# Performance work log

Hardware: AMD Instinct MI355X
Metric: run time of the kernel (lower is better)

Reference implementation:

```python
import jax, jax.numpy as jnp
import numpy as np

D = 768  # in_channels == out_channels (forced by residual + shared LayerNorm)
B, S = 8, 2048


def setup_inputs() -> dict:
    key = jax.random.key(0)
    ks = jax.random.split(key, 5)
    x = jax.random.normal(ks[0], (B, S, D), dtype=jnp.float32)
    # LayerNorm params
    ln_g = jnp.ones((D,), dtype=jnp.float32)
    ln_b = jnp.zeros((D,), dtype=jnp.float32)
    # Q/K linear params (torch Linear: y = x @ W.T + b)
    scale = 1.0 / np.sqrt(D)
    Wq = jax.random.uniform(ks[1], (D, D), jnp.float32, -scale, scale)
    bq = jax.random.uniform(ks[2], (D,), jnp.float32, -scale, scale)
    Wk = jax.random.uniform(ks[3], (D, D), jnp.float32, -scale, scale)
    bk = jax.random.uniform(ks[4], (D,), jnp.float32, -scale, scale)
    return {"x": x, "ln_g": ln_g, "ln_b": ln_b, "Wq": Wq, "bq": bq, "Wk": Wk, "bk": bk}


def _layernorm(x, g, b, eps=1e-5):
    mu = jnp.mean(x, axis=-1, keepdims=True)
    var = jnp.mean(jnp.square(x - mu), axis=-1, keepdims=True)
    return (x - mu) * jax.lax.rsqrt(var + eps) * g + b


def reference(x, ln_g, ln_b, Wq, bq, Wk, bk):
    origin = x
    xn = _layernorm(x, ln_g, ln_b)
    Q = xn @ Wq.T + bq  # [B,S,D]
    K = xn @ Wk.T + bk  # [B,S,D]
    scores = jnp.einsum('bsd,btd->bst', Q, K) / jnp.sqrt(jnp.asarray(D, x.dtype))
    attn = jax.nn.softmax(scores, axis=-1)  # [B,S,S]
    out = jnp.einsum('bst,btd->bsd', attn, origin) + origin
    # note: original then computes relu(layernorm(out)) but returns `out` (dead code)
    return out
```

## Files before the change

### kernel.cpp

```cpp
#include <hip/hip_runtime.h>

typedef __bf16 bf16;
typedef __bf16 v8bf __attribute__((ext_vector_type(8)));
typedef __bf16 v4bf __attribute__((ext_vector_type(4)));
typedef float  v4f  __attribute__((ext_vector_type(4)));

__device__ __forceinline__ void gload_lds16(const void* g, void* l) {
    __builtin_amdgcn_global_load_lds(
        (const __attribute__((address_space(1))) void*)g,
        (__attribute__((address_space(3))) void*)l, 16, 0, 0);
}

__global__ __launch_bounds__(256)
void ln_cast(const float* __restrict__ x, const float* __restrict__ g,
             const float* __restrict__ b, bf16* __restrict__ xn,
             bf16* __restrict__ xv, float* __restrict__ L)
{
    const long row = blockIdx.x;
    const float* xr = x + row * 768;
    const int tid = threadIdx.x;
    const int wave = tid >> 6, lane = tid & 63;

    if (row < 64) L[row * 256 + tid] = 0.0f;

    float a0 = xr[tid], a1 = xr[tid + 256], a2 = xr[tid + 512];
    float s = a0 + a1 + a2;
    #pragma unroll
    for (int off = 32; off; off >>= 1) s += __shfl_xor(s, off);
    __shared__ float sh[4], sh2[4];
    if (!lane) sh[wave] = s;
    __syncthreads();
    const float mu = (sh[0] + sh[1] + sh[2] + sh[3]) * (1.0f / 768.0f);

    float d0 = a0 - mu, d1 = a1 - mu, d2 = a2 - mu;
    float ss = d0 * d0 + d1 * d1 + d2 * d2;
    #pragma unroll
    for (int off = 32; off; off >>= 1) ss += __shfl_xor(ss, off);
    if (!lane) sh2[wave] = ss;
    __syncthreads();
    const float var = (sh2[0] + sh2[1] + sh2[2] + sh2[3]) * (1.0f / 768.0f);
    const float rstd = rsqrtf(var + 1e-5f);

    bf16* xnr = xn + row * 768;
    bf16* xvr = xv + row * 768;
    xnr[tid]       = (bf16)(d0 * rstd * g[tid]       + b[tid]);
    xnr[tid + 256] = (bf16)(d1 * rstd * g[tid + 256] + b[tid + 256]);
    xnr[tid + 512] = (bf16)(d2 * rstd * g[tid + 512] + b[tid + 512]);
    xvr[tid]       = (bf16)a0;
    xvr[tid + 256] = (bf16)a1;
    xvr[tid + 512] = (bf16)a2;
}

__global__ __launch_bounds__(256)
void cvt_w(const float* __restrict__ Wq, const float* __restrict__ Wk,
           bf16* __restrict__ Wcat)
{
    const int z = blockIdx.y;
    const float* src = z ? Wk : Wq;
    bf16* dst = Wcat + (long)z * 768 * 768;
    const int i = (blockIdx.x * 256 + threadIdx.x) * 4;
    const float4 v = *(const float4*)(src + i);
    v4bf o = {(bf16)v.x, (bf16)v.y, (bf16)v.z, (bf16)v.w};
    *(v4bf*)(dst + i) = o;
}

__global__ __launch_bounds__(256)
void transpose_bf(const bf16* __restrict__ in, bf16* __restrict__ outT)
{
    __shared__ __attribute__((aligned(16))) bf16 tile[64 * 64];
    const int t0 = blockIdx.x * 64, d0 = blockIdx.y * 64;
    in   += (long)blockIdx.z * 2048 * 768;
    outT += (long)blockIdx.z * 768 * 2048;
    const int tid = threadIdx.x;

    #pragma unroll
    for (int it = 0; it < 2; ++it) {
        const int lin = it * 256 + tid;
        const int r = lin >> 3;
        const int g = lin & 7;
        const int pg = g ^ (r & 7) ^ ((r >> 3) & 7);
        v8bf v = *(const v8bf*)(in + (long)(t0 + r) * 768 + d0 + g * 8);
        *(v8bf*)(tile + r * 64 + pg * 8) = v;
    }
    __syncthreads();
    #pragma unroll
    for (int it = 0; it < 2; ++it) {
        const int lin = it * 256 + tid;
        const int dd = lin >> 3;
        const int tb = lin & 7;
        v8bf o;
        #pragma unroll
        for (int j = 0; j < 8; ++j) {
            const int t = tb * 8 + j;
            const int pg = (dd >> 3) ^ (t & 7) ^ ((t >> 3) & 7);
            o[j] = tile[t * 64 + pg * 8 + (dd & 7)];
        }
        *(v8bf*)(outT + (long)(d0 + dd) * 2048 + t0 + tb * 8) = o;
    }
}

__global__ __launch_bounds__(256)
void gemm_qk(const bf16* __restrict__ A, const bf16* __restrict__ W,
             const float* __restrict__ bq, const float* __restrict__ bk,
             float qscale, bf16* __restrict__ Qb, bf16* __restrict__ Kb)
{
    __shared__ __attribute__((aligned(16))) bf16 As[2][128 * 32];
    __shared__ __attribute__((aligned(16))) bf16 Bs[2][128 * 32];

    const int bx = blockIdx.x;
    const int r = bx & 7, j = bx >> 3;
    const int m0 = (r * 16 + j / 12) * 128;
    const int n0 = (j % 12) * 128;

    const int tid = threadIdx.x, wave = tid >> 6, lane = tid & 63;
    const bf16* Ab = A + (long)m0 * 768;
    const bf16* Bb = W + (long)n0 * 768;

    const int lrow = lane >> 2;
    const int lk   = (lane & 3) * 8;
    const int wm = (wave >> 1) * 64, wn = (wave & 1) * 64;
    const int lr = lane & 15, lq = lane >> 4;

    v4f acc[4][4] = {};

    for (int kk = 0; kk < 768; kk += 64) {
        #pragma unroll
        for (int p = 0; p < 2; ++p)
            #pragma unroll
            for (int it = 0; it < 2; ++it) {
                const int c = it * 4 + wave;
                const int row = c * 16 + lrow;
                gload_lds16(Ab + (long)row * 768 + kk + p * 32 + lk,
                            (char*)As[p] + c * 1024);
                gload_lds16(Bb + (long)row * 768 + kk + p * 32 + lk,
                            (char*)Bs[p] + c * 1024);
            }
        __syncthreads();

        #pragma unroll
        for (int p = 0; p < 2; ++p) {
            v8bf af[4], bfr[4];
            #pragma unroll
            for (int i = 0; i < 4; ++i)
                af[i] = *(const v8bf*)(As[p] + (wm + i * 16 + lr) * 32 + lq * 8);
            #pragma unroll
            for (int jj = 0; jj < 4; ++jj)
                bfr[jj] = *(const v8bf*)(Bs[p] + (wn + jj * 16 + lr) * 32 + lq * 8);
            #pragma unroll
            for (int i = 0; i < 4; ++i)
                #pragma unroll
                for (int jj = 0; jj < 4; ++jj)
                    acc[i][jj] = __builtin_amdgcn_mfma_f32_16x16x32_bf16(
                        af[i], bfr[jj], acc[i][jj], 0, 0, 0);
        }
        __syncthreads();
    }

    const bool isQ = (n0 < 768);
    const float* bias = isQ ? bq : bk;
    const float sc = isQ ? qscale : 1.0f;
    bf16* C = isQ ? Qb : Kb;
    const int c0 = isQ ? n0 : n0 - 768;

    #pragma unroll
    for (int i = 0; i < 4; ++i) {
        #pragma unroll
        for (int rr = 0; rr < 4; ++rr) {
            const int row = m0 + wm + i * 16 + lq * 4 + rr;
            #pragma unroll
            for (int jj = 0; jj < 4; ++jj) {
                const int col = c0 + wn + jj * 16 + lr;
                C[(long)row * 768 + col] = (bf16)((acc[i][jj][rr] + bias[col]) * sc);
            }
        }
    }
}

__global__ __launch_bounds__(512, 2)
void gemm_scores(const bf16* __restrict__ Q, const bf16* __restrict__ K,
                 bf16* __restrict__ E, float* __restrict__ L)
{
    __shared__ __attribute__((aligned(16))) bf16 lds[3][24576];

    const int bx = blockIdx.x;
    const int batch = bx & 7, j = bx >> 3;
    const int mt = j >> 3, nt = j & 7;
    const int m0 = mt * 128, n0 = nt * 256;

    const bf16* Ag = Q + (long)batch * 2048 * 768 + (long)m0 * 768;
    const bf16* Bg = K + (long)batch * 2048 * 768 + (long)n0 * 768;
    bf16* C = E + (long)batch * 2048 * 2048;
    float* Lb = L + (long)batch * 2048;

    const int tid = threadIdx.x, wv = tid >> 6, lane = tid & 63;
    const int wr = wv >> 2, wc = wv & 3;
    const int lr = lane & 15, lq = lane >> 4;

    auto stageA = [&](int slot, int kk, int a) {
        const int lin = a * 64 + lane;
        const int r = lin >> 3;
        const int ck = (lin & 7) ^ (r & 7);
        gload_lds16(Ag + (long)r * 768 + kk + ck * 8,
                    (char*)lds[slot] + a * 1024);
    };
    auto stageB = [&](int slot, int kk, int b) {
        const int lin = b * 64 + lane;
        const int r = lin >> 3;
        const int ck = (lin & 7) ^ (r & 7);
        gload_lds16(Bg + (long)r * 768 + kk + ck * 8,
                    (char*)lds[slot] + 16384 + b * 1024);
    };

    v4f acc[4][4] = {};
    const int NT = 12;

    #pragma unroll
    for (int tt = 0; tt < 2; ++tt) {
        stageA(tt, tt * 64, wv * 2 + 0);
        stageA(tt, tt * 64, wv * 2 + 1);
        #pragma unroll
        for (int l = 0; l < 4; ++l) stageB(tt, tt * 64, wv * 4 + l);
    }
    asm volatile("s_waitcnt vmcnt(6)" ::: "memory");
    __builtin_amdgcn_s_barrier();

    for (int t = 0; t < NT; ++t) {
        const int cur = t % 3;
        const int nxt = (t + 2) % 3;
        const int kk2 = (t + 2) * 64;
        const bf16* As = lds[cur];
        const bf16* Bs = lds[cur] + 8192;
        const bool pre = (t + 2 < NT);

        v8bf af[4][2], bfr[2][2];
        #pragma unroll
        for (int i = 0; i < 4; ++i) {
            const int row = wr * 64 + i * 16 + lr;
            #pragma unroll
            for (int s = 0; s < 2; ++s)
                af[i][s] = *(const v8bf*)(As + row * 64 +
                                          (((s * 4 + lq) ^ (row & 7)) << 3));
        }
        #pragma unroll
        for (int jn = 0; jn < 2; ++jn) {
            const int row = wc * 64 + jn * 16 + lr;
            #pragma unroll
            for (int s = 0; s < 2; ++s)
                bfr[jn][s] = *(const v8bf*)(Bs + row * 64 +
                                            (((s * 4 + lq) ^ (row & 7)) << 3));
        }
        if (pre) {
            stageA(nxt, kk2, wv * 2 + 0);
            stageA(nxt, kk2, wv * 2 + 1);
            stageB(nxt, kk2, wv * 4 + 0);
        }
        __builtin_amdgcn_s_barrier();
        asm volatile("s_waitcnt lgkmcnt(0)" ::: "memory");
        __builtin_amdgcn_s_setprio(1);
        #pragma unroll
        for (int s = 0; s < 2; ++s)
            #pragma unroll
            for (int i = 0; i < 4; ++i)
                #pragma unroll
                for (int jn = 0; jn < 2; ++jn)
                    acc[i][jn] = __builtin_amdgcn_mfma_f32_16x16x32_bf16(
                        af[i][s], bfr[jn][s], acc[i][jn], 0, 0, 0);
        __builtin_amdgcn_s_setprio(0);
        __builtin_amdgcn_s_barrier();

        #pragma unroll
        for (int jn = 0; jn < 2; ++jn) {
            const int row = wc * 64 + (jn + 2) * 16 + lr;
            #pragma unroll
            for (int s = 0; s < 2; ++s)
                bfr[jn][s] = *(const v8bf*)(Bs + row * 64 +
                                            (((s * 4 + lq) ^ (row & 7)) << 3));
        }
        if (pre) {
            stageB(nxt, kk2, wv * 4 + 1);
            stageB(nxt, kk2, wv * 4 + 2);
            stageB(nxt, kk2, wv * 4 + 3);
        }
        __builtin_amdgcn_s_barrier();
        asm volatile("s_waitcnt lgkmcnt(0)" ::: "memory");
        __builtin_amdgcn_s_setprio(1);
        #pragma unroll
        for (int s = 0; s < 2; ++s)
            #pragma unroll
            for (int i = 0; i < 4; ++i)
                #pragma unroll
                for (int jn = 0; jn < 2; ++jn)
                    acc[i][jn + 2] = __builtin_amdgcn_mfma_f32_16x16x32_bf16(
                        af[i][s], bfr[jn][s], acc[i][jn + 2], 0, 0, 0);
        __builtin_amdgcn_s_setprio(0);
        if (t < NT - 2)       asm volatile("s_waitcnt vmcnt(6)" ::: "memory");
        else if (t == NT - 2) asm volatile("s_waitcnt vmcnt(0)" ::: "memory");
        __builtin_amdgcn_s_barrier();
    }

    #pragma unroll
    for (int i = 0; i < 4; ++i) {
        #pragma unroll
        for (int rr = 0; rr < 4; ++rr) {
            const int row = m0 + wr * 64 + i * 16 + lq * 4 + rr;
            float e[4], rs = 0.f;
            #pragma unroll
            for (int jn = 0; jn < 4; ++jn) {
                e[jn] = __expf(acc[i][jn][rr]);
                rs += e[jn];
            }
            #pragma unroll
            for (int off = 1; off < 16; off <<= 1) rs += __shfl_xor(rs, off);
            if (lr == 0) atomicAdd(&Lb[row], rs);
            #pragma unroll
            for (int jn = 0; jn < 4; ++jn) {
                const int col = n0 + wc * 64 + jn * 16 + lr;
                C[(long)row * 2048 + col] = (bf16)e[jn];
            }
        }
    }
}

__global__ __launch_bounds__(512, 2)
void gemm_pv(const bf16* __restrict__ P, const bf16* __restrict__ VT,
             const float* __restrict__ L, const float* __restrict__ Xres,
             float* __restrict__ Out)
{
    __shared__ __attribute__((aligned(16))) bf16 lds[2][32768];

    const int bx = blockIdx.x;
    const int batch = bx & 7, j = bx >> 3;
    const int m0 = (j >> 1) * 128;
    const int n0 = (j & 1) * 384;

    const bf16* Ag = P  + (long)batch * 2048 * 2048 + (long)m0 * 2048;
    const bf16* Bg = VT + (long)batch * 768 * 2048  + (long)n0 * 2048;
    const float* Lb = L + (long)batch * 2048;
    const float* Xr = Xres + (long)batch * 2048 * 768;
    float* O = Out + (long)batch * 2048 * 768;

    const int tid = threadIdx.x, wv = tid >> 6, lane = tid & 63;
    const int wr = wv >> 2, wc = wv & 3;
    const int lr = lane & 15, lq = lane >> 4;

    auto stageA = [&](int slot, int kk, int a) {
        const int lin = a * 64 + lane;
        const int r = lin >> 3;
        const int ck = (lin & 7) ^ (r & 7);
        gload_lds16(Ag + (long)r * 2048 + kk + ck * 8,
                    (char*)lds[slot] + a * 1024);
    };
    auto stageB = [&](int slot, int kk, int b) {
        const int lin = b * 64 + lane;
        const int r = lin >> 3;
        const int ck = (lin & 7) ^ (r & 7);
        gload_lds16(Bg + (long)r * 2048 + kk + ck * 8,
                    (char*)lds[slot] + 16384 + b * 1024);
    };

    v4f acc[4][6] = {};
    const int NT = 32;

    stageA(0, 0, wv * 2 + 0);
    stageA(0, 0, wv * 2 + 1);
    #pragma unroll
    for (int l = 0; l < 6; ++l) stageB(0, 0, wv * 6 + l);
    asm volatile("s_waitcnt vmcnt(0)" ::: "memory");
    __builtin_amdgcn_s_barrier();

    for (int t = 0; t < NT; ++t) {
        const int cur = t & 1, nxt = cur ^ 1;
        const int kk1 = (t + 1) * 64;
        const bf16* As = lds[cur];
        const bf16* Bs = lds[cur] + 8192;
        const bool pre = (t + 1 < NT);

        v8bf af[4][2], bfr[3][2];
        #pragma unroll
        for (int i = 0; i < 4; ++i) {
            const int row = wr * 64 + i * 16 + lr;
            #pragma unroll
            for (int s = 0; s < 2; ++s)
                af[i][s] = *(const v8bf*)(As + row * 64 +
                                          (((s * 4 + lq) ^ (row & 7)) << 3));
        }
        #pragma unroll
        for (int jn = 0; jn < 3; ++jn) {
            const int row = wc * 96 + jn * 16 + lr;
            #pragma unroll
            for (int s = 0; s < 2; ++s)
                bfr[jn][s] = *(const v8bf*)(Bs + row * 64 +
                                            (((s * 4 + lq) ^ (row & 7)) << 3));
        }
        if (pre) {
            stageA(nxt, kk1, wv * 2 + 0);
            stageA(nxt, kk1, wv * 2 + 1);
            stageB(nxt, kk1, wv * 6 + 0);
            stageB(nxt, kk1, wv * 6 + 1);
        }
        __builtin_amdgcn_s_barrier();
        asm volatile("s_waitcnt lgkmcnt(0)" ::: "memory");
        __builtin_amdgcn_s_setprio(1);
        #pragma unroll
        for (int s = 0; s < 2; ++s)
            #pragma unroll
            for (int i = 0; i < 4; ++i)
                #pragma unroll
                for (int jn = 0; jn < 3; ++jn)
                    acc[i][jn] = __builtin_amdgcn_mfma_f32_16x16x32_bf16(
                        af[i][s], bfr[jn][s], acc[i][jn], 0, 0, 0);
        __builtin_amdgcn_s_setprio(0);
        __builtin_amdgcn_s_barrier();

        #pragma unroll
        for (int jn = 0; jn < 3; ++jn) {
            const int row = wc * 96 + (jn + 3) * 16 + lr;
            #pragma unroll
            for (int s = 0; s < 2; ++s)
                bfr[jn][s] = *(const v8bf*)(Bs + row * 64 +
                                            (((s * 4 + lq) ^ (row & 7)) << 3));
        }
        if (pre) {
            stageB(nxt, kk1, wv * 6 + 2);
            stageB(nxt, kk1, wv * 6 + 3);
            stageB(nxt, kk1, wv * 6 + 4);
            stageB(nxt, kk1, wv * 6 + 5);
        }
        __builtin_amdgcn_s_barrier();
        asm volatile("s_waitcnt lgkmcnt(0)" ::: "memory");
        __builtin_amdgcn_s_setprio(1);
        #pragma unroll
        for (int s = 0; s < 2; ++s)
            #pragma unroll
            for (int i = 0; i < 4; ++i)
                #pragma unroll
                for (int jn = 0; jn < 3; ++jn)
                    acc[i][jn + 3] = __builtin_amdgcn_mfma_f32_16x16x32_bf16(
                        af[i][s], bfr[jn][s], acc[i][jn + 3], 0, 0, 0);
        __builtin_amdgcn_s_setprio(0);
        if (pre) asm volatile("s_waitcnt vmcnt(0)" ::: "memory");
        __builtin_amdgcn_s_barrier();
    }

    #pragma unroll
    for (int i = 0; i < 4; ++i) {
        #pragma unroll
        for (int rr = 0; rr < 4; ++rr) {
            const int row = m0 + wr * 64 + i * 16 + lq * 4 + rr;
            const float invL = 1.0f / Lb[row];
            #pragma unroll
            for (int jn = 0; jn < 6; ++jn) {
                const int col = n0 + wc * 96 + jn * 16 + lr;
                const long idx = (long)row * 768 + col;
                O[idx] = acc[i][jn][rr] * invL + Xr[idx];
            }
        }
    }
}

extern "C" void kernel_launch(void* const* d_in, const int* in_sizes, int n_in,
                              void* d_out, int out_size, void* d_ws, size_t ws_size,
                              hipStream_t stream)
{
    const float* x    = (const float*)d_in[0];
    const float* ln_g = (const float*)d_in[1];
    const float* ln_b = (const float*)d_in[2];
    const float* Wq   = (const float*)d_in[3];
    const float* bq   = (const float*)d_in[4];
    const float* Wk   = (const float*)d_in[5];
    const float* bk   = (const float*)d_in[6];
    float* out = (float*)d_out;

    const long R = 8L * 2048;
    char* ws = (char*)d_ws;
    size_t off = 0;
    auto take = [&](size_t bytes) -> char* {
        char* p = ws + off;
        off += (bytes + 255) & ~(size_t)255;
        return p;
    };
    bf16*  xn   = (bf16*)take(R * 768 * 2);
    bf16*  xv   = (bf16*)take(R * 768 * 2);
    bf16*  Qb   = (bf16*)take(R * 768 * 2);
    bf16*  Kb   = (bf16*)take(R * 768 * 2);
    bf16*  Wcat = (bf16*)take(1536L * 768 * 2);
    float* Lrow = (float*)take(R * 4);
    bf16*  Sc   = (bf16*)take(8L * 2048 * 2048 * 2);

    ln_cast<<<R, 256, 0, stream>>>(x, ln_g, ln_b, xn, xv, Lrow);
    cvt_w<<<dim3(576, 2), 256, 0, stream>>>(Wq, Wk, Wcat);

    const float qscale = 0.036084391824351615f;
    gemm_qk<<<1536, 256, 0, stream>>>(xn, Wcat, bq, bk, qscale, Qb, Kb);

    bf16* xvT = xn;
    transpose_bf<<<dim3(32, 12, 8), 256, 0, stream>>>(xv, xvT);

    gemm_scores<<<1024, 512, 0, stream>>>(Qb, Kb, Sc, Lrow);
    gemm_pv<<<256, 512, 0, stream>>>(Sc, xvT, Lrow, x, out);
}
```

Measured before the change: 335.7 us.

## Restructure score and PV GEMMs into 4-stage half-K ping-pong MFMA pipelines

Both attention GEMMs now stage 32-wide K slices into a 4-slot LDS ring and interleave fragment reads, async global-to-LDS loads and MFMA quarters, so the next fragments are loaded while the current ones compute. The scores kernel also doubles its M tile to 256, which halves the grid and gives each wave an 8x4 accumulator tile for more operand reuse. The intent is to hide LDS and global latency and cut per-tile load traffic. In exchange register pressure rises and the grid gets smaller, which may lower occupancy or leave CUs underused.

```diff
diff --git a/kernel.cpp b/kernel.cpp
--- a/kernel.cpp
+++ b/kernel.cpp
@@ -10,6 +10,8 @@
         (const __attribute__((address_space(1))) void*)g,
         (__attribute__((address_space(3))) void*)l, 16, 0, 0);
 }
+
+#define MFMA16(a, b, c) __builtin_amdgcn_mfma_f32_16x16x32_bf16((a), (b), (c), 0, 0, 0)
 
 __global__ __launch_bounds__(256)
 void ln_cast(const float* __restrict__ x, const float* __restrict__ g,
@@ -150,8 +152,7 @@
             for (int i = 0; i < 4; ++i)
                 #pragma unroll
                 for (int jj = 0; jj < 4; ++jj)
-                    acc[i][jj] = __builtin_amdgcn_mfma_f32_16x16x32_bf16(
-                        af[i], bfr[jj], acc[i][jj], 0, 0, 0);
+                    acc[i][jj] = MFMA16(af[i], bfr[jj], acc[i][jj]);
         }
         __syncthreads();
     }
@@ -180,12 +181,11 @@
 void gemm_scores(const bf16* __restrict__ Q, const bf16* __restrict__ K,
                  bf16* __restrict__ E, float* __restrict__ L)
 {
-    __shared__ __attribute__((aligned(16))) bf16 lds[3][24576];
+    __shared__ __attribute__((aligned(16))) bf16 lds[4][16384];
 
     const int bx = blockIdx.x;
     const int batch = bx & 7, j = bx >> 3;
-    const int mt = j >> 3, nt = j & 7;
-    const int m0 = mt * 128, n0 = nt * 256;
+    const int m0 = (j >> 3) * 256, n0 = (j & 7) * 256;
 
     const bf16* Ag = Q + (long)batch * 2048 * 768 + (long)m0 * 768;
     const bf16* Bg = K + (long)batch * 2048 * 768 + (long)n0 * 768;
@@ -196,113 +196,108 @@
     const int wr = wv >> 2, wc = wv & 3;
     const int lr = lane & 15, lq = lane >> 4;
 
-    auto stageA = [&](int slot, int kk, int a) {
-        const int lin = a * 64 + lane;
-        const int r = lin >> 3;
-        const int ck = (lin & 7) ^ (r & 7);
-        gload_lds16(Ag + (long)r * 768 + kk + ck * 8,
-                    (char*)lds[slot] + a * 1024);
-    };
-    auto stageB = [&](int slot, int kk, int b) {
-        const int lin = b * 64 + lane;
-        const int r = lin >> 3;
-        const int ck = (lin & 7) ^ (r & 7);
-        gload_lds16(Bg + (long)r * 768 + kk + ck * 8,
-                    (char*)lds[slot] + 16384 + b * 1024);
-    };
-
-    v4f acc[4][4] = {};
+    auto stageA = [&](int h, int a) {
+        const int lin = (wv * 2 + a) * 64 + lane;
+        const int r = lin >> 2, pc = lin & 3;
+        gload_lds16(Ag + (long)r * 768 + h * 32 + ((pc ^ (r & 3)) << 3),
+                    (char*)lds[h & 3] + lin * 16);
+    };
+    auto stageB = [&](int h, int a) {
+        const int lin = (wv * 2 + a) * 64 + lane;
+        const int r = lin >> 2, pc = lin & 3;
+        gload_lds16(Bg + (long)r * 768 + h * 32 + ((pc ^ (r & 3)) << 3),
+                    (char*)lds[h & 3] + 16384 + lin * 16);
+    };
+    auto rdA = [&](int h, int mf) -> v8bf {
+        const int r = wr * 128 + mf * 16 + lr;
+        return *(const v8bf*)(lds[h & 3] + r * 32 + ((lq ^ (r & 3)) << 3));
+    };
+    auto rdB = [&](int h, int nf) -> v8bf {
+        const int r = wc * 64 + nf * 16 + lr;
+        return *(const v8bf*)(lds[h & 3] + 8192 + r * 32 + ((lq ^ (r & 3)) << 3));
+    };
+
+    v8bf a0[4], a1[4], b0[4], b1[4];
+    v4f acc[8][4] = {};
     const int NT = 12;
 
-    #pragma unroll
-    for (int tt = 0; tt < 2; ++tt) {
-        stageA(tt, tt * 64, wv * 2 + 0);
-        stageA(tt, tt * 64, wv * 2 + 1);
-        #pragma unroll
-        for (int l = 0; l < 4; ++l) stageB(tt, tt * 64, wv * 4 + l);
-    }
-    asm volatile("s_waitcnt vmcnt(6)" ::: "memory");
+    stageA(0, 0); stageA(0, 1); stageB(0, 0); stageB(0, 1);
+    stageA(1, 0); stageA(1, 1); stageB(1, 0); stageB(1, 1);
+    asm volatile("s_waitcnt vmcnt(4)" ::: "memory");
     __builtin_amdgcn_s_barrier();
+    #pragma unroll
+    for (int i = 0; i < 4; ++i) a0[i] = rdA(0, i);
+    #pragma unroll
+    for (int jn = 0; jn < 4; ++jn) b0[jn] = rdB(0, jn);
 
     for (int t = 0; t < NT; ++t) {
-        const int cur = t % 3;
-        const int nxt = (t + 2) % 3;
-        const int kk2 = (t + 2) * 64;
-        const bf16* As = lds[cur];
-        const bf16* Bs = lds[cur] + 8192;
-        const bool pre = (t + 2 < NT);
-
-        v8bf af[4][2], bfr[2][2];
-        #pragma unroll
-        for (int i = 0; i < 4; ++i) {
-            const int row = wr * 64 + i * 16 + lr;
-            #pragma unroll
-            for (int s = 0; s < 2; ++s)
-                af[i][s] = *(const v8bf*)(As + row * 64 +
-                                          (((s * 4 + lq) ^ (row & 7)) << 3));
-        }
-        #pragma unroll
-        for (int jn = 0; jn < 2; ++jn) {
-            const int row = wc * 64 + jn * 16 + lr;
-            #pragma unroll
-            for (int s = 0; s < 2; ++s)
-                bfr[jn][s] = *(const v8bf*)(Bs + row * 64 +
-                                            (((s * 4 + lq) ^ (row & 7)) << 3));
-        }
+        const int h0 = 2 * t, h1 = 2 * t + 1, h2 = 2 * t + 2, h3 = 2 * t + 3;
+        const bool pre = (t + 1 < NT);
+
+        #pragma unroll
+        for (int i = 0; i < 4; ++i) a1[i] = rdA(h0, 4 + i);
+        if (pre) { stageA(h2, 0); stageA(h2, 1); }
+        __builtin_amdgcn_s_setprio(1);
+        #pragma unroll
+        for (int i = 0; i < 4; ++i)
+            #pragma unroll
+            for (int jn = 0; jn < 4; ++jn)
+                acc[i][jn] = MFMA16(a0[i], b0[jn], acc[i][jn]);
+        __builtin_amdgcn_s_setprio(0);
+        asm volatile("s_waitcnt vmcnt(2)" ::: "memory");
+        __builtin_amdgcn_s_barrier();
+
+        #pragma unroll
+        for (int i = 0; i < 4; ++i) a0[i] = rdA(h1, i);
+        #pragma unroll
+        for (int jn = 0; jn < 4; ++jn) b1[jn] = rdB(h1, jn);
+        if (pre) { stageB(h2, 0); stageB(h2, 1); }
+        __builtin_amdgcn_s_setprio(1);
+        #pragma unroll
+        for (int i = 0; i < 4; ++i)
+            #pragma unroll
+            for (int jn = 0; jn < 4; ++jn)
+                acc[4 + i][jn] = MFMA16(a1[i], b0[jn], acc[4 + i][jn]);
+        __builtin_amdgcn_s_setprio(0);
+        asm volatile("" ::: "memory");
+        __builtin_amdgcn_s_barrier();
+
+        #pragma unroll
+        for (int i = 0; i < 4; ++i) a1[i] = rdA(h1, 4 + i);
+        if (pre) { stageA(h3, 0); stageA(h3, 1); }
+        __builtin_amdgcn_s_setprio(1);
+        #pragma unroll
+        for (int i = 0; i < 4; ++i)
+            #pragma unroll
+            for (int jn = 0; jn < 4; ++jn)
+                acc[i][jn] = MFMA16(a0[i], b1[jn], acc[i][jn]);
+        __builtin_amdgcn_s_setprio(0);
+        asm volatile("s_waitcnt vmcnt(2)" ::: "memory");
+        __builtin_amdgcn_s_barrier();
+
         if (pre) {
-            stageA(nxt, kk2, wv * 2 + 0);
-            stageA(nxt, kk2, wv * 2 + 1);
-            stageB(nxt, kk2, wv * 4 + 0);
-        }
-        __builtin_amdgcn_s_barrier();
-        asm volatile("s_waitcnt lgkmcnt(0)" ::: "memory");
-        __builtin_amdgcn_s_setprio(1);
-        #pragma unroll
-        for (int s = 0; s < 2; ++s)
-            #pragma unroll
-            for (int i = 0; i < 4; ++i)
-                #pragma unroll
-                for (int jn = 0; jn < 2; ++jn)
-                    acc[i][jn] = __builtin_amdgcn_mfma_f32_16x16x32_bf16(
-                        af[i][s], bfr[jn][s], acc[i][jn], 0, 0, 0);
-        __builtin_amdgcn_s_setprio(0);
-        __builtin_amdgcn_s_barrier();
-
-        #pragma unroll
-        for (int jn = 0; jn < 2; ++jn) {
-            const int row = wc * 64 + (jn + 2) * 16 + lr;
-            #pragma unroll
-            for (int s = 0; s < 2; ++s)
-                bfr[jn][s] = *(const v8bf*)(Bs + row * 64 +
-                                            (((s * 4 + lq) ^ (row & 7)) << 3));
-        }
-        if (pre) {
-            stageB(nxt, kk2, wv * 4 + 1);
-            stageB(nxt, kk2, wv * 4 + 2);
-            stageB(nxt, kk2, wv * 4 + 3);
-        }
-        __builtin_amdgcn_s_barrier();
-        asm volatile("s_waitcnt lgkmcnt(0)" ::: "memory");
-        __builtin_amdgcn_s_setprio(1);
-        #pragma unroll
-        for (int s = 0; s < 2; ++s)
-            #pragma unroll
-            for (int i = 0; i < 4; ++i)
-                #pragma unroll
-                for (int jn = 0; jn < 2; ++jn)
-                    acc[i][jn + 2] = __builtin_amdgcn_mfma_f32_16x16x32_bf16(
-                        af[i][s], bfr[jn][s], acc[i][jn + 2], 0, 0, 0);
-        __builtin_amdgcn_s_setprio(0);
-        if (t < NT - 2)       asm volatile("s_waitcnt vmcnt(6)" ::: "memory");
-        else if (t == NT - 2) asm volatile("s_waitcnt vmcnt(0)" ::: "memory");
-        __builtin_amdgcn_s_barrier();
-    }
-
-    #pragma unroll
-    for (int i = 0; i < 4; ++i) {
+            #pragma unroll
+            for (int i = 0; i < 4; ++i) a0[i] = rdA(h2, i);
+            #pragma unroll
+            for (int jn = 0; jn < 4; ++jn) b0[jn] = rdB(h2, jn);
+            stageB(h3, 0); stageB(h3, 1);
+        }
+        __builtin_amdgcn_s_setprio(1);
+        #pragma unroll
+        for (int i = 0; i < 4; ++i)
+            #pragma unroll
+            for (int jn = 0; jn < 4; ++jn)
+                acc[4 + i][jn] = MFMA16(a1[i], b1[jn], acc[4 + i][jn]);
+        __builtin_amdgcn_s_setprio(0);
+        asm volatile("" ::: "memory");
+        __builtin_amdgcn_s_barrier();
+    }
+
+    #pragma unroll
+    for (int i = 0; i < 8; ++i) {
         #pragma unroll
         for (int rr = 0; rr < 4; ++rr) {
-            const int row = m0 + wr * 64 + i * 16 + lq * 4 + rr;
+            const int row = m0 + wr * 128 + i * 16 + lq * 4 + rr;
             float e[4], rs = 0.f;
             #pragma unroll
             for (int jn = 0; jn < 4; ++jn) {
@@ -326,7 +321,7 @@
              const float* __restrict__ L, const float* __restrict__ Xres,
              float* __restrict__ Out)
 {
-    __shared__ __attribute__((aligned(16))) bf16 lds[2][32768];
+    __shared__ __attribute__((aligned(16))) bf16 lds[4][16384];
 
     const int bx = blockIdx.x;
     const int batch = bx & 7, j = bx >> 3;
@@ -343,102 +338,100 @@
     const int wr = wv >> 2, wc = wv & 3;
     const int lr = lane & 15, lq = lane >> 4;
 
-    auto stageA = [&](int slot, int kk, int a) {
-        const int lin = a * 64 + lane;
-        const int r = lin >> 3;
-        const int ck = (lin & 7) ^ (r & 7);
-        gload_lds16(Ag + (long)r * 2048 + kk + ck * 8,
-                    (char*)lds[slot] + a * 1024);
-    };
-    auto stageB = [&](int slot, int kk, int b) {
-        const int lin = b * 64 + lane;
-        const int r = lin >> 3;
-        const int ck = (lin & 7) ^ (r & 7);
-        gload_lds16(Bg + (long)r * 2048 + kk + ck * 8,
-                    (char*)lds[slot] + 16384 + b * 1024);
-    };
-
+    auto stageA = [&](int h) {
+        const int lin = wv * 64 + lane;
+        const int r = lin >> 2, pc = lin & 3;
+        gload_lds16(Ag + (long)r * 2048 + h * 32 + ((pc ^ (r & 3)) << 3),
+                    (char*)lds[h & 3] + lin * 16);
+    };
+    auto stageB = [&](int h, int a) {
+        const int lin = (wv * 3 + a) * 64 + lane;
+        const int r = lin >> 2, pc = lin & 3;
+        gload_lds16(Bg + (long)r * 2048 + h * 32 + ((pc ^ (r & 3)) << 3),
+                    (char*)lds[h & 3] + 8192 + lin * 16);
+    };
+    auto rdA = [&](int h, int mf) -> v8bf {
+        const int r = wr * 64 + mf * 16 + lr;
+        return *(const v8bf*)(lds[h & 3] + r * 32 + ((lq ^ (r & 3)) << 3));
+    };
+    auto rdB = [&](int h, int nf) -> v8bf {
+        const int r = wc * 96 + nf * 16 + lr;
+        return *(const v8bf*)(lds[h & 3] + 4096 + r * 32 + ((lq ^ (r & 3)) << 3));
+    };
+
+    v8bf a0[4], a1[4], bL[3], bH[3];
     v4f acc[4][6] = {};
     const int NT = 32;
 
-    stageA(0, 0, wv * 2 + 0);
-    stageA(0, 0, wv * 2 + 1);
-    #pragma unroll
-    for (int l = 0; l < 6; ++l) stageB(0, 0, wv * 6 + l);
-    asm volatile("s_waitcnt vmcnt(0)" ::: "memory");
+    stageA(0); stageB(0, 0); stageB(0, 1); stageB(0, 2);
+    stageA(1); stageB(1, 0); stageB(1, 1); stageB(1, 2);
+    asm volatile("s_waitcnt vmcnt(4)" ::: "memory");
     __builtin_amdgcn_s_barrier();
+    #pragma unroll
+    for (int i = 0; i < 4; ++i) a0[i] = rdA(0, i);
+    #pragma unroll
+    for (int jn = 0; jn < 3; ++jn) bL[jn] = rdB(0, jn);
 
     for (int t = 0; t < NT; ++t) {
-        const int cur = t & 1, nxt = cur ^ 1;
-        const int kk1 = (t + 1) * 64;
-        const bf16* As = lds[cur];
-        const bf16* Bs = lds[cur] + 8192;
+        const int h0 = 2 * t, h1 = 2 * t + 1, h2 = 2 * t + 2, h3 = 2 * t + 3;
         const bool pre = (t + 1 < NT);
 
-        v8bf af[4][2], bfr[3][2];
-        #pragma unroll
-        for (int i = 0; i < 4; ++i) {
-            const int row = wr * 64 + i * 16 + lr;
-            #pragma unroll
-            for (int s = 0; s < 2; ++s)
-                af[i][s] = *(const v8bf*)(As + row * 64 +
-                                          (((s * 4 + lq) ^ (row & 7)) << 3));
-        }
-        #pragma unroll
-        for (int jn = 0; jn < 3; ++jn) {
-            const int row = wc * 96 + jn * 16 + lr;
-            #pragma unroll
-            for (int s = 0; s < 2; ++s)
-                bfr[jn][s] = *(const v8bf*)(Bs + row * 64 +
-                                            (((s * 4 + lq) ^ (row & 7)) << 3));
-        }
+        #pragma unroll
+        for (int jn = 0; jn < 3; ++jn) bH[jn] = rdB(h0, 3 + jn);
+        if (pre) { stageA(h2); stageB(h2, 0); }
+        __builtin_amdgcn_s_setprio(1);
+        #pragma unroll
+        for (int i = 0; i < 4; ++i)
+            #pragma unroll
+            for (int jn = 0; jn < 3; ++jn)
+                acc[i][jn] = MFMA16(a0[i], bL[jn], acc[i][jn]);
+        __builtin_amdgcn_s_setprio(0);
+        asm volatile("s_waitcnt vmcnt(2)" ::: "memory");
+        __builtin_amdgcn_s_barrier();
+
+        #pragma unroll
+        for (int i = 0; i < 4; ++i) a1[i] = rdA(h1, i);
+        #pragma unroll
+        for (int jn = 0; jn < 3; ++jn) bL[jn] = rdB(h1, jn);
+        if (pre) { stageB(h2, 1); stageB(h2, 2); }
+        __builtin_amdgcn_s_setprio(1);
+        #pragma unroll
+        for (int i = 0; i < 4; ++i)
+            #pragma unroll
+            for (int jn = 0; jn < 3; ++jn)
+                acc[i][3 + jn] = MFMA16(a0[i], bH[jn], acc[i][3 + jn]);
+        __builtin_amdgcn_s_setprio(0);
+        asm volatile("" ::: "memory");
+        __builtin_amdgcn_s_barrier();
+
+        #pragma unroll
+        for (int jn = 0; jn < 3; ++jn) bH[jn] = rdB(h1, 3 + jn);
+        if (pre) { stageA(h3); stageB(h3, 0); }
+        __builtin_amdgcn_s_setprio(1);
+        #pragma unroll
+        for (int i = 0; i < 4; ++i)
+            #pragma unroll
+            for (int jn = 0; jn < 3; ++jn)
+                acc[i][jn] = MFMA16(a1[i], bL[jn], acc[i][jn]);
+        __builtin_amdgcn_s_setprio(0);
+        asm volatile("s_waitcnt vmcnt(2)" ::: "memory");
+        __builtin_amdgcn_s_barrier();
+
         if (pre) {
-            stageA(nxt, kk1, wv * 2 + 0);
-            stageA(nxt, kk1, wv * 2 + 1);
-            stageB(nxt, kk1, wv * 6 + 0);
-            stageB(nxt, kk1, wv * 6 + 1);
-        }
-        __builtin_amdgcn_s_barrier();
-        asm volatile("s_waitcnt lgkmcnt(0)" ::: "memory");
-        __builtin_amdgcn_s_setprio(1);
-        #pragma unroll
-        for (int s = 0; s < 2; ++s)
-            #pragma unroll
-            for (int i = 0; i < 4; ++i)
-                #pragma unroll
-                for (int jn = 0; jn < 3; ++jn)
-                    acc[i][jn] = __builtin_amdgcn_mfma_f32_16x16x32_bf16(
-                        af[i][s], bfr[jn][s], acc[i][jn], 0, 0, 0);
-        __builtin_amdgcn_s_setprio(0);
-        __builtin_amdgcn_s_barrier();
-
-        #pragma unroll
-        for (int jn = 0; jn < 3; ++jn) {
-            const int row = wc * 96 + (jn + 3) * 16 + lr;
-            #pragma unroll
-            for (int s = 0; s < 2; ++s)
-                bfr[jn][s] = *(const v8bf*)(Bs + row * 64 +
-                                            (((s * 4 + lq) ^ (row & 7)) << 3));
-        }
-        if (pre) {
-            stageB(nxt, kk1, wv * 6 + 2);
-            stageB(nxt, kk1, wv * 6 + 3);
-            stageB(nxt, kk1, wv * 6 + 4);
-            stageB(nxt, kk1, wv * 6 + 5);
-        }
-        __builtin_amdgcn_s_barrier();
-        asm volatile("s_waitcnt lgkmcnt(0)" ::: "memory");
-        __builtin_amdgcn_s_setprio(1);
-        #pragma unroll
-        for (int s = 0; s < 2; ++s)
-            #pragma unroll
-            for (int i = 0; i < 4; ++i)
-                #pragma unroll
-                for (int jn = 0; jn < 3; ++jn)
-                    acc[i][jn + 3] = __builtin_amdgcn_mfma_f32_16x16x32_bf16(
-                        af[i][s], bfr[jn][s], acc[i][jn + 3], 0, 0, 0);
-        __builtin_amdgcn_s_setprio(0);
-        if (pre) asm volatile("s_waitcnt vmcnt(0)" ::: "memory");
+            #pragma unroll
+            for (int i = 0; i < 4; ++i) a0[i] = rdA(h2, i);
+            #pragma unroll
+            for (int jn = 0; jn < 3; ++jn) bL[jn] = rdB(h2, jn);
+            stageB(h3, 1); stageB(h3, 2);
+        }
+        __builtin_amdgcn_s_setprio(1);
+        #pragma unroll
+        for (int i = 0; i < 4; ++i)
+            #pragma unroll
+            for (int jn = 0; jn < 3; ++jn)
+                acc[i][3 + jn] = MFMA16(a1[i], bH[jn], acc[i][3 + jn]);
+        __builtin_amdgcn_s_setprio(0);
+        asm volatile("" ::: "memory");
         __builtin_amdgcn_s_barrier();
     }
 
@@ -496,6 +489,6 @@
     bf16* xvT = xn;
     transpose_bf<<<dim3(32, 12, 8), 256, 0, stream>>>(xv, xvT);
 
-    gemm_scores<<<1024, 512, 0, stream>>>(Qb, Kb, Sc, Lrow);
+    gemm_scores<<<512, 512, 0, stream>>>(Qb, Kb, Sc, Lrow);
     gemm_pv<<<256, 512, 0, stream>>>(Sc, xvT, Lrow, x, out);
 }
```

Result: faster. 316.3 us (-5.8%).
